# Performance work log

Hardware: AMD Instinct MI355X
Metric: run time of the kernel (lower is better)

The kernel has to match this reference:

```python
import jax, jax.numpy as jnp
import numpy as np

FEATS = 64
POS = 3
EDGE_ATTR = 4
M_DIM = 16
N_LAYERS = 3
EDGE_IN = 2 * FEATS + EDGE_ATTR + 1  # 133


def setup_inputs() -> dict:
    key = jax.random.key(0)
    ks = jax.random.split(key, 20)
    N, E = 50000, 800000
    x = jax.random.normal(ks[0], (N, FEATS + POS), dtype=jnp.float32)
    edge_index = jax.random.randint(ks[1], (2, E), 0, N, dtype=jnp.int64)
    edge_attr = jax.random.normal(ks[2], (E, EDGE_ATTR), dtype=jnp.float32)
    s = 0.02
    L = N_LAYERS
    inp = {
        "x": x, "edge_index": edge_index, "edge_attr": edge_attr,
        # edge_mlp: Linear(EDGE_IN, 2*EDGE_IN) -> SiLU -> Linear(2*EDGE_IN, M_DIM) -> SiLU
        "edge_w1": jax.random.normal(ks[3], (L, EDGE_IN, 2 * EDGE_IN), dtype=jnp.float32) * s,
        "edge_b1": jnp.zeros((L, 2 * EDGE_IN), dtype=jnp.float32),
        "edge_w2": jax.random.normal(ks[4], (L, 2 * EDGE_IN, M_DIM), dtype=jnp.float32) * s,
        "edge_b2": jnp.zeros((L, M_DIM), dtype=jnp.float32),
        # coors_mlp: Linear(M, 4M) -> SiLU -> Linear(4M, 1)
        "coors_w1": jax.random.normal(ks[5], (L, M_DIM, 4 * M_DIM), dtype=jnp.float32) * s,
        "coors_b1": jnp.zeros((L, 4 * M_DIM), dtype=jnp.float32),
        "coors_w2": jax.random.normal(ks[6], (L, 4 * M_DIM, 1), dtype=jnp.float32) * s,
        "coors_b2": jnp.zeros((L, 1), dtype=jnp.float32),
        # node_mlp: Linear(FEATS+M, 2*FEATS) -> SiLU -> Linear(2*FEATS, FEATS)
        "node_w1": jax.random.normal(ks[7], (L, FEATS + M_DIM, 2 * FEATS), dtype=jnp.float32) * s,
        "node_b1": jnp.zeros((L, 2 * FEATS), dtype=jnp.float32),
        "node_w2": jax.random.normal(ks[8], (L, 2 * FEATS, FEATS), dtype=jnp.float32) * s,
        "node_b2": jnp.zeros((L, FEATS), dtype=jnp.float32),
    }
    return inp


def _egnn_layer(x, edge_index, edge_attr,
                ew1, eb1, ew2, eb2, cw1, cb1, cw2, cb2, nw1, nb1, nw2, nb2):
    N = x.shape[0]
    feats, coors = x[:, :FEATS], x[:, FEATS:]
    src, dst = edge_index[0], edge_index[1]
    rel_coors = coors[src] - coors[dst]                       # [E, 3]
    rel_dist = jnp.sum(rel_coors ** 2, axis=-1, keepdims=True)  # [E, 1]
    ea = jnp.concatenate([edge_attr, rel_dist], axis=-1)      # [E, EDGE_ATTR+1]
    # PyG default flow source_to_target: x_i = x[dst], x_j = x[src]
    edge_in = jnp.concatenate([feats[dst], feats[src], ea], axis=-1)  # [E, EDGE_IN]
    h = jax.nn.silu(edge_in @ ew1 + eb1)
    m_ij = jax.nn.silu(h @ ew2 + eb2)                         # [E, M_DIM]
    coor_w = jax.nn.silu(m_ij @ cw1 + cb1) @ cw2 + cb2        # [E, 1]
    # aggregate (default 'add') over destination nodes
    m_i = jax.ops.segment_sum(m_ij, dst, num_segments=N)      # [N, M_DIM]
    coor_wi = jax.ops.segment_sum(coor_w, dst, num_segments=N)  # [N, 1]
    coor_ri = jax.ops.segment_sum(rel_coors, dst, num_segments=N)  # [N, 3]
    coors_out = coors + coor_wi * coor_ri
    node_in = jnp.concatenate([feats, m_i], axis=-1)
    hidden = jax.nn.silu(node_in @ nw1 + nb1) @ nw2 + nb2
    hidden_out = hidden + feats
    return jnp.concatenate([hidden_out, coors_out], axis=-1)


def reference(x, edge_index, edge_attr,
              edge_w1, edge_b1, edge_w2, edge_b2,
              coors_w1, coors_b1, coors_w2, coors_b2,
              node_w1, node_b1, node_w2, node_b2):
    for l in range(N_LAYERS):
        x = _egnn_layer(x, edge_index, edge_attr,
                        edge_w1[l], edge_b1[l], edge_w2[l], edge_b2[l],
                        coors_w1[l], coors_b1[l], coors_w2[l], coors_b2[l],
                        node_w1[l], node_b1[l], node_w2[l], node_b2[l])
    return x
```

## Files before the change

kernel.cpp:

```cpp
#include <hip/hip_runtime.h>
#include <hip/hip_bf16.h>

#define XDIM 67
#define EIN_D 133
#define H1 266
#define KP 160
#define KP_E 168
#define JP 320
#define JP_H 328
#define MSTR 40
#define EPB 48

typedef __attribute__((ext_vector_type(8))) short bf16x8;
typedef __attribute__((ext_vector_type(4))) float f32x4;
typedef __attribute__((ext_vector_type(2))) float f32x2;
typedef __attribute__((ext_vector_type(2))) __bf16 b16x2;

__device__ __forceinline__ float silu_f(float x) {
    return x * __builtin_amdgcn_rcpf(1.f + __expf(-x));
}

__device__ __forceinline__ unsigned short bf16_rne(float f) {
    unsigned int u = __float_as_uint(f);
    u += 0x7fffu + ((u >> 16) & 1u);
    return (unsigned short)(u >> 16);
}
__device__ __forceinline__ float bf16_to_f(unsigned short h) {
    return __uint_as_float(((unsigned int)h) << 16);
}
__device__ __forceinline__ unsigned int packbf2(float a, float b) {
    b16x2 c = __builtin_convertvector((f32x2){a, b}, b16x2);
    unsigned int u; __builtin_memcpy(&u, &c, 4); return u;
}

__global__ void copy_zero_kernel(const float* __restrict__ src, float* __restrict__ dst,
                                 int n, float* __restrict__ z, int nz) {
    int n4 = n >> 2, nz4 = nz >> 2;
    const float4* s4 = (const float4*)src;
    float4* d4 = (float4*)dst;
    float4* z4 = (float4*)z;
    for (int i = blockIdx.x * blockDim.x + threadIdx.x; i < n4; i += gridDim.x * blockDim.x)
        d4[i] = s4[i];
    for (int i = blockIdx.x * blockDim.x + threadIdx.x; i < nz4; i += gridDim.x * blockDim.x)
        z4[i] = make_float4(0.f, 0.f, 0.f, 0.f);
    if (blockIdx.x == 0 && threadIdx.x == 0) {
        for (int i = n4 * 4; i < n; ++i) dst[i] = src[i];
        for (int i = nz4 * 4; i < nz; ++i) z[i] = 0.f;
    }
}

__global__ void prep_w1t(const float* __restrict__ ew1, unsigned short* __restrict__ whi,
                         unsigned short* __restrict__ wlo) {
    int idx = blockIdx.x * 256 + threadIdx.x;
    if (idx >= 3 * JP * KP) return;
    int l = idx / (JP * KP);
    int rem = idx - l * JP * KP;
    int j = rem / KP, k = rem - (rem / KP) * KP;
    float w = (j < H1 && k < EIN_D) ? ew1[((size_t)l * EIN_D + k) * H1 + j] : 0.f;
    unsigned short h = bf16_rne(w);
    whi[idx] = h;
    wlo[idx] = bf16_rne(w - bf16_to_f(h));
}

__global__ void prep_w2t(const float* __restrict__ ew2, unsigned short* __restrict__ w2tg) {
    int idx = blockIdx.x * 256 + threadIdx.x;
    if (idx >= 3 * 16 * JP_H) return;
    int l = idx / (16 * JP_H);
    int rem = idx - l * 16 * JP_H;
    int c = rem / JP_H, j = rem - (rem / JP_H) * JP_H;
    float w = (j < H1) ? ew2[((size_t)l * H1 + j) * 16 + c] : 0.f;
    unsigned short h = bf16_rne(w);
    w2tg[((size_t)l * 2 + 0) * 16 * JP_H + c * JP_H + j] = h;
    w2tg[((size_t)l * 2 + 1) * 16 * JP_H + c * JP_H + j] = bf16_rne(w - bf16_to_f(h));
}

__global__ void prep_b1(const float* __restrict__ b1, float* __restrict__ b1p) {
    int idx = blockIdx.x * 256 + threadIdx.x;
    if (idx >= 3 * JP) return;
    int l = idx / JP, j = idx - (idx / JP) * JP;
    b1p[idx] = (j < H1) ? b1[l * H1 + j] : 0.f;
}

__global__ void prep_cw1t(const float* __restrict__ cw1, unsigned short* __restrict__ cw1t) {
    int idx = blockIdx.x * 256 + threadIdx.x;
    if (idx >= 3 * 64 * 32) return;
    int l = idx / (64 * 32);
    int rem = idx - l * 64 * 32;
    int j = rem >> 5, c = rem & 31;
    cw1t[idx] = (c < 16) ? bf16_rne(cw1[(size_t)l * 16 * 64 + c * 64 + j]) : (unsigned short)0;
}

__device__ __forceinline__ void store_feats(unsigned short* __restrict__ ein_hi,
                                            unsigned short* __restrict__ ein_lo,
                                            int er, int c0, const float* v) {
    unsigned int dh01 = packbf2(v[0], v[1]), dh23 = packbf2(v[2], v[3]);
    unsigned int sh01 = packbf2(v[4], v[5]), sh23 = packbf2(v[6], v[7]);
    float dl0 = v[0] - __uint_as_float(dh01 << 16);
    float dl1 = v[1] - __uint_as_float(dh01 & 0xffff0000u);
    float dl2 = v[2] - __uint_as_float(dh23 << 16);
    float dl3 = v[3] - __uint_as_float(dh23 & 0xffff0000u);
    float sl0 = v[4] - __uint_as_float(sh01 << 16);
    float sl1 = v[5] - __uint_as_float(sh01 & 0xffff0000u);
    float sl2 = v[6] - __uint_as_float(sh23 << 16);
    float sl3 = v[7] - __uint_as_float(sh23 & 0xffff0000u);
    uint2 u;
    u.x = dh01; u.y = dh23;
    *(uint2*)&ein_hi[er * KP_E + c0] = u;
    u.x = packbf2(dl0, dl1); u.y = packbf2(dl2, dl3);
    *(uint2*)&ein_lo[er * KP_E + c0] = u;
    u.x = sh01; u.y = sh23;
    *(uint2*)&ein_hi[er * KP_E + 64 + c0] = u;
    u.x = packbf2(sl0, sl1); u.y = packbf2(sl2, sl3);
    *(uint2*)&ein_lo[er * KP_E + 64 + c0] = u;
}

__global__ __launch_bounds__(256, 4) void edge_kernel(
    const float* __restrict__ x,
    const int* __restrict__ eidx,
    const float* __restrict__ eattr,
    const unsigned short* __restrict__ w1hi,
    const unsigned short* __restrict__ w1lo,
    const float* __restrict__ b1p,
    const unsigned short* __restrict__ w2tg,
    const float* __restrict__ b2,
    const unsigned short* __restrict__ cw1t,
    const float* __restrict__ cb1,
    const float* __restrict__ cw2, const float* __restrict__ cb2,
    float* __restrict__ m_i, float* __restrict__ cri, float* __restrict__ cwi,
    int E, int N)
{
    __shared__ __align__(16) unsigned short uA[2 * EPB * KP_E];
    __shared__ __align__(16) unsigned short mij_bf[EPB * MSTR];
    __shared__ float relc[EPB][4];
    __shared__ int dstl[EPB];

    unsigned short* ein_hi = uA;
    unsigned short* ein_lo = uA + EPB * KP_E;
    unsigned short* h_hi   = uA;

    const int tid = threadIdx.x;
    const int lane = tid & 63;
    const int w = tid >> 6;
    const int ge0 = blockIdx.x * EPB;
    const int r16 = lane & 15, g4 = lane >> 4;

    const int c0 = r16 * 4;
    const int erA = w * 12 + g4, erB = erA + 4, erC = erA + 8;
    const int geA = ge0 + erA, geB = ge0 + erB, geC = ge0 + erC;
    const int sA = (geA < E) ? eidx[geA] : 0, dA = (geA < E) ? eidx[E + geA] : 0;
    const int sB = (geB < E) ? eidx[geB] : 0, dB = (geB < E) ? eidx[E + geB] : 0;
    const int sC = (geC < E) ? eidx[geC] : 0, dC = (geC < E) ? eidx[E + geC] : 0;
    float vA[8], vB[8], vC[8];
    {
        const float* p;
        p = x + (size_t)dA * XDIM + c0; vA[0] = p[0]; vA[1] = p[1]; vA[2] = p[2]; vA[3] = p[3];
        p = x + (size_t)sA * XDIM + c0; vA[4] = p[0]; vA[5] = p[1]; vA[6] = p[2]; vA[7] = p[3];
        p = x + (size_t)dB * XDIM + c0; vB[0] = p[0]; vB[1] = p[1]; vB[2] = p[2]; vB[3] = p[3];
        p = x + (size_t)sB * XDIM + c0; vB[4] = p[0]; vB[5] = p[1]; vB[6] = p[2]; vB[7] = p[3];
        p = x + (size_t)dC * XDIM + c0; vC[0] = p[0]; vC[1] = p[1]; vC[2] = p[2]; vC[3] = p[3];
        p = x + (size_t)sC * XDIM + c0; vC[4] = p[0]; vC[5] = p[1]; vC[6] = p[2]; vC[7] = p[3];
    }

    if (tid < EPB) {
        int e = tid, ge = ge0 + e;
        if (ge < E) {
            int s = eidx[ge];
            int d = eidx[E + ge];
            dstl[e] = d;
            const float* xs = x + (size_t)s * XDIM;
            const float* xd = x + (size_t)d * XDIM;
            float r0 = xs[64] - xd[64], r1 = xs[65] - xd[65], r2 = xs[66] - xd[66];
            relc[e][0] = r0; relc[e][1] = r1; relc[e][2] = r2;
            float dist = r0 * r0 + r1 * r1 + r2 * r2;
            unsigned short hh = bf16_rne(dist);
            ein_hi[e * KP_E + 132] = hh;
            ein_lo[e * KP_E + 132] = bf16_rne(dist - bf16_to_f(hh));
        } else {
            dstl[e] = 0;
            relc[e][0] = relc[e][1] = relc[e][2] = 0.f;
            ein_hi[e * KP_E + 132] = 0;
            ein_lo[e * KP_E + 132] = 0;
        }
    }
    if (tid >= 64) {
        int t = tid - 64;
        int e = t >> 2, c = t & 3, ge = ge0 + e;
        float a = (ge < E) ? eattr[(size_t)ge * 4 + c] : 0.f;
        unsigned short hh = bf16_rne(a);
        ein_hi[e * KP_E + 128 + c] = hh;
        ein_lo[e * KP_E + 128 + c] = bf16_rne(a - bf16_to_f(hh));
    }
    for (int t = tid; t < EPB * 27; t += 256) {
        int e = t / 27, c = 133 + (t - (t / 27) * 27);
        ein_hi[e * KP_E + c] = 0;
        ein_lo[e * KP_E + c] = 0;
    }
    if (tid < 192) {
        int e = tid >> 2, q = tid & 3;
        uint2 zz; zz.x = 0u; zz.y = 0u;
        *(uint2*)&mij_bf[e * MSTR + 16 + q * 4] = zz;
    }

    store_feats(ein_hi, ein_lo, erA, c0, vA);
    store_feats(ein_hi, ein_lo, erB, c0, vB);
    store_feats(ein_hi, ein_lo, erC, c0, vC);
    __syncthreads();

    const int jt0 = w * 5;

    f32x4 acc[5][3];
#pragma unroll
    for (int a = 0; a < 5; ++a)
#pragma unroll
        for (int b = 0; b < 3; ++b) acc[a][b] = (f32x4){0.f, 0.f, 0.f, 0.f};

    __builtin_amdgcn_s_setprio(1);
#pragma unroll
    for (int kk = 0; kk < 5; ++kk) {
        const int ko = kk * 32 + g4 * 8;
        bf16x8 ah[3], al[3];
#pragma unroll
        for (int et = 0; et < 3; ++et) {
            ah[et] = *(const bf16x8*)&ein_hi[(et * 16 + r16) * KP_E + ko];
            al[et] = *(const bf16x8*)&ein_lo[(et * 16 + r16) * KP_E + ko];
        }
#pragma unroll
        for (int j5 = 0; j5 < 5; ++j5) {
            const size_t wo = (size_t)((jt0 + j5) * 16 + r16) * KP + ko;
            bf16x8 bh = *(const bf16x8*)&w1hi[wo];
            bf16x8 bl = *(const bf16x8*)&w1lo[wo];
#pragma unroll
            for (int et = 0; et < 3; ++et) {
                acc[j5][et] = __builtin_amdgcn_mfma_f32_16x16x32_bf16(bh, ah[et], acc[j5][et], 0, 0, 0);
                acc[j5][et] = __builtin_amdgcn_mfma_f32_16x16x32_bf16(bl, ah[et], acc[j5][et], 0, 0, 0);
                acc[j5][et] = __builtin_amdgcn_mfma_f32_16x16x32_bf16(bh, al[et], acc[j5][et], 0, 0, 0);
            }
        }
    }
    __builtin_amdgcn_s_setprio(0);

    float4 b1v[5];
#pragma unroll
    for (int j5 = 0; j5 < 5; ++j5)
        b1v[j5] = *(const float4*)&b1p[(jt0 + j5) * 16 + g4 * 4];

    __syncthreads();

#pragma unroll
    for (int j5 = 0; j5 < 5; ++j5) {
#pragma unroll
        for (int et = 0; et < 3; ++et) {
            f32x4 a = acc[j5][et];
            float h0 = silu_f(a[0] + b1v[j5].x);
            float h1 = silu_f(a[1] + b1v[j5].y);
            float h2 = silu_f(a[2] + b1v[j5].z);
            float h3 = silu_f(a[3] + b1v[j5].w);
            uint2 uu;
            uu.x = packbf2(h0, h1);
            uu.y = packbf2(h2, h3);
            *(uint2*)&h_hi[(et * 16 + r16) * JP_H + (jt0 + j5) * 16 + g4 * 4] = uu;
        }
    }
    __syncthreads();

    if (w < 3) {
        f32x4 acc2 = (f32x4){0.f, 0.f, 0.f, 0.f};
        const unsigned short* hrow = &h_hi[(w * 16 + r16) * JP_H];
        const unsigned short* w2h = &w2tg[(size_t)r16 * JP_H];
        const unsigned short* w2l = &w2tg[(size_t)(16 + r16) * JP_H];
#pragma unroll
        for (int kk = 0; kk < 10; ++kk) {
            const int ko = kk * 32 + g4 * 8;
            bf16x8 hf = *(const bf16x8*)&hrow[ko];
            bf16x8 wh = *(const bf16x8*)&w2h[ko];
            bf16x8 wl = *(const bf16x8*)&w2l[ko];
            acc2 = __builtin_amdgcn_mfma_f32_16x16x32_bf16(hf, wh, acc2, 0, 0, 0);
            acc2 = __builtin_amdgcn_mfma_f32_16x16x32_bf16(hf, wl, acc2, 0, 0, 0);
        }
        float b2v = b2[r16];
#pragma unroll
        for (int r = 0; r < 4; ++r) {
            int e = w * 16 + g4 * 4 + r;
            float m = silu_f(acc2[r] + b2v);
            mij_bf[e * MSTR + r16] = bf16_rne(m);
            if (ge0 + e < E) atomicAdd(&m_i[(size_t)dstl[e] * 16 + r16], m);
        }
    }
    __syncthreads();

    if (w < 3) {
        bf16x8 afrag = *(const bf16x8*)&mij_bf[(w * 16 + r16) * MSTR + g4 * 8];
        f32x4 cacc[4];
#pragma unroll
        for (int jt = 0; jt < 4; ++jt) {
            bf16x8 bfrag = *(const bf16x8*)&cw1t[(jt * 16 + r16) * 32 + g4 * 8];
            cacc[jt] = __builtin_amdgcn_mfma_f32_16x16x32_bf16(afrag, bfrag,
                        (f32x4){0.f, 0.f, 0.f, 0.f}, 0, 0, 0);
        }
        float pw0 = 0.f, pw1 = 0.f, pw2 = 0.f, pw3 = 0.f;
#pragma unroll
        for (int jt = 0; jt < 4; ++jt) {
            float cb = cb1[jt * 16 + r16];
            float cw = cw2[jt * 16 + r16];
            pw0 += silu_f(cacc[jt][0] + cb) * cw;
            pw1 += silu_f(cacc[jt][1] + cb) * cw;
            pw2 += silu_f(cacc[jt][2] + cb) * cw;
            pw3 += silu_f(cacc[jt][3] + cb) * cw;
        }
#pragma unroll
        for (int s = 1; s < 16; s <<= 1) {
            pw0 += __shfl_xor(pw0, s, 16);
            pw1 += __shfl_xor(pw1, s, 16);
            pw2 += __shfl_xor(pw2, s, 16);
            pw3 += __shfl_xor(pw3, s, 16);
        }
        if (r16 == 0) {
            float cb2v = cb2[0];
            int e = w * 16 + g4 * 4;
            relc[e + 0][3] = pw0 + cb2v;
            relc[e + 1][3] = pw1 + cb2v;
            relc[e + 2][3] = pw2 + cb2v;
            relc[e + 3][3] = pw3 + cb2v;
        }
    }
    __syncthreads();

    if (tid < EPB * 4) {
        int e = tid >> 2, c = tid & 3;
        if (ge0 + e < E) {
            int d = dstl[e];
            if (c < 3) atomicAdd(&cri[(size_t)d * 3 + c], relc[e][c]);
            else       atomicAdd(&cwi[d], relc[e][3]);
        }
    }
}

__global__ __launch_bounds__(256) void node_kernel(
    const float* xin,
    float* __restrict__ m_i,
    float* __restrict__ cri,
    float* __restrict__ cwi,
    const float* __restrict__ nw1, const float* __restrict__ nb1,
    const float* __restrict__ nw2, const float* __restrict__ nb2,
    float* xout, int N)
{
    __shared__ __align__(16) float nin[2][80];
    __shared__ __align__(16) float hid[2][128];
    const int half = threadIdx.x >> 7, r = threadIdx.x & 127;
    const int n = blockIdx.x * 2 + half;
    const bool on = (n < N);

    if (on) {
        if (r < 64)      nin[half][r] = xin[(size_t)n * XDIM + r];
        else if (r < 80) nin[half][r] = m_i[(size_t)n * 16 + (r - 64)];
    }
    __syncthreads();
    if (on) {
        float p0 = 0.f, p1 = 0.f, p2 = 0.f, p3 = 0.f;
#pragma unroll
        for (int k = 0; k < 80; k += 16) {
            float4 a0 = *(const float4*)&nin[half][k];
            float4 a1 = *(const float4*)&nin[half][k + 4];
            float4 a2 = *(const float4*)&nin[half][k + 8];
            float4 a3 = *(const float4*)&nin[half][k + 12];
            p0 += a0.x * nw1[(k + 0) * 128 + r] + a0.y * nw1[(k + 1) * 128 + r]
                + a0.z * nw1[(k + 2) * 128 + r] + a0.w * nw1[(k + 3) * 128 + r];
            p1 += a1.x * nw1[(k + 4) * 128 + r] + a1.y * nw1[(k + 5) * 128 + r]
                + a1.z * nw1[(k + 6) * 128 + r] + a1.w * nw1[(k + 7) * 128 + r];
            p2 += a2.x * nw1[(k + 8) * 128 + r] + a2.y * nw1[(k + 9) * 128 + r]
                + a2.z * nw1[(k + 10) * 128 + r] + a2.w * nw1[(k + 11) * 128 + r];
            p3 += a3.x * nw1[(k + 12) * 128 + r] + a3.y * nw1[(k + 13) * 128 + r]
                + a3.z * nw1[(k + 14) * 128 + r] + a3.w * nw1[(k + 15) * 128 + r];
        }
        hid[half][r] = silu_f(nb1[r] + ((p0 + p1) + (p2 + p3)));
    }
    __syncthreads();
    if (on) {
        if (r < 64) {
            float p0 = 0.f, p1 = 0.f, p2 = 0.f, p3 = 0.f;
#pragma unroll
            for (int k = 0; k < 128; k += 16) {
                float4 a0 = *(const float4*)&hid[half][k];
                float4 a1 = *(const float4*)&hid[half][k + 4];
                float4 a2 = *(const float4*)&hid[half][k + 8];
                float4 a3 = *(const float4*)&hid[half][k + 12];
                p0 += a0.x * nw2[(k + 0) * 64 + r] + a0.y * nw2[(k + 1) * 64 + r]
                    + a0.z * nw2[(k + 2) * 64 + r] + a0.w * nw2[(k + 3) * 64 + r];
                p1 += a1.x * nw2[(k + 4) * 64 + r] + a1.y * nw2[(k + 5) * 64 + r]
                    + a1.z * nw2[(k + 6) * 64 + r] + a1.w * nw2[(k + 7) * 64 + r];
                p2 += a2.x * nw2[(k + 8) * 64 + r] + a2.y * nw2[(k + 9) * 64 + r]
                    + a2.z * nw2[(k + 10) * 64 + r] + a2.w * nw2[(k + 11) * 64 + r];
                p3 += a3.x * nw2[(k + 12) * 64 + r] + a3.y * nw2[(k + 13) * 64 + r]
                    + a3.z * nw2[(k + 14) * 64 + r] + a3.w * nw2[(k + 15) * 64 + r];
            }
            xout[(size_t)n * XDIM + r] = nb2[r] + ((p0 + p1) + (p2 + p3)) + nin[half][r];
        } else if (r < 67) {
            int c = r - 64;
            xout[(size_t)n * XDIM + r] =
                xin[(size_t)n * XDIM + r] + cwi[n] * cri[(size_t)n * 3 + c];
        }
    }
    __syncthreads();
    if (on) {
        if (r < 16)      m_i[(size_t)n * 16 + r] = 0.f;
        else if (r < 19) cri[(size_t)n * 3 + (r - 16)] = 0.f;
        else if (r == 19) cwi[n] = 0.f;
    }
}

extern "C" void kernel_launch(void* const* d_in, const int* in_sizes, int n_in,
                              void* d_out, int out_size, void* d_ws, size_t ws_size,
                              hipStream_t stream) {
    const float* x     = (const float*)d_in[0];
    const int*   eidx  = (const int*)d_in[1];
    const float* eattr = (const float*)d_in[2];
    const float* ew1   = (const float*)d_in[3];
    const float* eb1   = (const float*)d_in[4];
    const float* ew2   = (const float*)d_in[5];
    const float* eb2   = (const float*)d_in[6];
    const float* cw1   = (const float*)d_in[7];
    const float* cb1   = (const float*)d_in[8];
    const float* cw2   = (const float*)d_in[9];
    const float* cb2   = (const float*)d_in[10];
    const float* nw1   = (const float*)d_in[11];
    const float* nb1   = (const float*)d_in[12];
    const float* nw2   = (const float*)d_in[13];
    const float* nb2   = (const float*)d_in[14];

    const int N = in_sizes[0] / XDIM;
    const int E = in_sizes[1] / 2;

    float* acc  = (float*)d_ws;
    float* m_i  = acc;
    float* cri  = acc + (size_t)N * 16;
    float* cwi  = acc + (size_t)N * 19;
    float* b1p  = acc + (size_t)N * 20;
    unsigned short* w1hi = (unsigned short*)(b1p + (size_t)3 * JP);
    unsigned short* w1lo = w1hi + (size_t)3 * JP * KP;
    unsigned short* w2tg = w1lo + (size_t)3 * JP * KP;
    unsigned short* cw1t = w2tg + (size_t)3 * 2 * 16 * JP_H;

    float* xwork = (float*)d_out;

    copy_zero_kernel<<<2048, 256, 0, stream>>>(x, xwork, N * XDIM, acc, N * 20);
    prep_w1t<<<(3 * JP * KP + 255) / 256, 256, 0, stream>>>(ew1, w1hi, w1lo);
    prep_w2t<<<(3 * 16 * JP_H + 255) / 256, 256, 0, stream>>>(ew2, w2tg);
    prep_b1<<<(3 * JP + 255) / 256, 256, 0, stream>>>(eb1, b1p);
    prep_cw1t<<<(3 * 64 * 32 + 255) / 256, 256, 0, stream>>>(cw1, cw1t);

    for (int l = 0; l < 3; ++l) {
        edge_kernel<<<(E + EPB - 1) / EPB, 256, 0, stream>>>(
            xwork, eidx, eattr,
            w1hi + (size_t)l * JP * KP, w1lo + (size_t)l * JP * KP,
            b1p + (size_t)l * JP,
            w2tg + (size_t)l * 2 * 16 * JP_H,
            eb2 + (size_t)l * 16,
            cw1t + (size_t)l * 64 * 32,
            cb1 + (size_t)l * 64,
            cw2 + (size_t)l * 64, cb2 + l,
            m_i, cri, cwi, E, N);
        node_kernel<<<(N + 1) / 2, 256, 0, stream>>>(
            xwork, m_i, cri, cwi,
            nw1 + (size_t)l * 80 * 128, nb1 + (size_t)l * 128,
            nw2 + (size_t)l * 128 * 64, nb2 + (size_t)l * 64,
            xwork, N);
    }
}
```

Before: 1.761 ms.

## Sort edges by destination and pre-reduce per-destination runs before atomics

Adds a counting sort of edges by destination node (histogram, single-block scan, scatter into a permutation) once per forward pass. The edge kernel now processes edges in that permuted order and replaces its per-edge atomics with a block-local segmented reduction over runs of equal destination, issuing one atomic per run and channel. The aim is to cut global atomic traffic and contention, and to improve locality of the destination-row gathers. The cost is an extra indirection for edge indices and attributes, the sort kernels including a serial single-block scan, and message sums now built from bf16-rounded m_ij values instead of fp32, which loses precision.

```diff
diff --git a/kernel.cpp b/kernel.cpp
--- a/kernel.cpp
+++ b/kernel.cpp
@@ -49,12 +49,48 @@
     }
 }
 
+__global__ void hist_kernel(const int* __restrict__ eidx, int* __restrict__ cnt, int E) {
+    int i = blockIdx.x * 256 + threadIdx.x;
+    if (i < E) atomicAdd(&cnt[eidx[E + i]], 1);
+}
+
+__global__ __launch_bounds__(256) void scan_kernel(const int* __restrict__ cnt,
+                                                   int* __restrict__ off, int N) {
+    __shared__ int ssum[256];
+    const int tid = threadIdx.x;
+    const int strip = (N + 255) / 256;
+    const int s = tid * strip;
+    const int e = (s + strip < N) ? (s + strip) : N;
+    int acc = 0;
+    for (int i = s; i < e; ++i) acc += cnt[i];
+    ssum[tid] = acc;
+    __syncthreads();
+    for (int d = 1; d < 256; d <<= 1) {
+        int v = (tid >= d) ? ssum[tid - d] : 0;
+        __syncthreads();
+        ssum[tid] += v;
+        __syncthreads();
+    }
+    int base = (tid > 0) ? ssum[tid - 1] : 0;
+    for (int i = s; i < e; ++i) { int c = cnt[i]; off[i] = base; base += c; }
+}
+
+__global__ void scatter_kernel(const int* __restrict__ eidx, int* __restrict__ off,
+                               int* __restrict__ perm, int E) {
+    int i = blockIdx.x * 256 + threadIdx.x;
+    if (i < E) {
+        int d = eidx[E + i];
+        int pos = atomicAdd(&off[d], 1);
+        perm[pos] = i;
+    }
+}
+
 __global__ void prep_w1t(const float* __restrict__ ew1, unsigned short* __restrict__ whi,
                          unsigned short* __restrict__ wlo) {
     int idx = blockIdx.x * 256 + threadIdx.x;
     if (idx >= 3 * JP * KP) return;
     int l = idx / (JP * KP);
-    int rem = idx - l * JP * KP;
+    int rem = idx - l * (JP * KP);
     int j = rem / KP, k = rem - (rem / KP) * KP;
     float w = (j < H1 && k < EIN_D) ? ew1[((size_t)l * EIN_D + k) * H1 + j] : 0.f;
     unsigned short h = bf16_rne(w);
@@ -66,7 +102,7 @@
     int idx = blockIdx.x * 256 + threadIdx.x;
     if (idx >= 3 * 16 * JP_H) return;
     int l = idx / (16 * JP_H);
-    int rem = idx - l * 16 * JP_H;
+    int rem = idx - l * (16 * JP_H);
     int c = rem / JP_H, j = rem - (rem / JP_H) * JP_H;
     float w = (j < H1) ? ew2[((size_t)l * H1 + j) * 16 + c] : 0.f;
     unsigned short h = bf16_rne(w);
@@ -85,7 +121,7 @@
     int idx = blockIdx.x * 256 + threadIdx.x;
     if (idx >= 3 * 64 * 32) return;
     int l = idx / (64 * 32);
-    int rem = idx - l * 64 * 32;
+    int rem = idx - l * (64 * 32);
     int j = rem >> 5, c = rem & 31;
     cw1t[idx] = (c < 16) ? bf16_rne(cw1[(size_t)l * 16 * 64 + c * 64 + j]) : (unsigned short)0;
 }
@@ -117,6 +153,7 @@
 __global__ __launch_bounds__(256, 4) void edge_kernel(
     const float* __restrict__ x,
     const int* __restrict__ eidx,
+    const int* __restrict__ perm,
     const float* __restrict__ eattr,
     const unsigned short* __restrict__ w1hi,
     const unsigned short* __restrict__ w1lo,
@@ -147,9 +184,12 @@
     const int c0 = r16 * 4;
     const int erA = w * 12 + g4, erB = erA + 4, erC = erA + 8;
     const int geA = ge0 + erA, geB = ge0 + erB, geC = ge0 + erC;
-    const int sA = (geA < E) ? eidx[geA] : 0, dA = (geA < E) ? eidx[E + geA] : 0;
-    const int sB = (geB < E) ? eidx[geB] : 0, dB = (geB < E) ? eidx[E + geB] : 0;
-    const int sC = (geC < E) ? eidx[geC] : 0, dC = (geC < E) ? eidx[E + geC] : 0;
+    const int peA = (geA < E) ? perm[geA] : 0;
+    const int peB = (geB < E) ? perm[geB] : 0;
+    const int peC = (geC < E) ? perm[geC] : 0;
+    const int sA = (geA < E) ? eidx[peA] : 0, dA = (geA < E) ? eidx[E + peA] : 0;
+    const int sB = (geB < E) ? eidx[peB] : 0, dB = (geB < E) ? eidx[E + peB] : 0;
+    const int sC = (geC < E) ? eidx[peC] : 0, dC = (geC < E) ? eidx[E + peC] : 0;
     float vA[8], vB[8], vC[8];
     {
         const float* p;
@@ -164,8 +204,9 @@
     if (tid < EPB) {
         int e = tid, ge = ge0 + e;
         if (ge < E) {
-            int s = eidx[ge];
-            int d = eidx[E + ge];
+            int pe = perm[ge];
+            int s = eidx[pe];
+            int d = eidx[E + pe];
             dstl[e] = d;
             const float* xs = x + (size_t)s * XDIM;
             const float* xd = x + (size_t)d * XDIM;
@@ -176,7 +217,7 @@
             ein_hi[e * KP_E + 132] = hh;
             ein_lo[e * KP_E + 132] = bf16_rne(dist - bf16_to_f(hh));
         } else {
-            dstl[e] = 0;
+            dstl[e] = -1;
             relc[e][0] = relc[e][1] = relc[e][2] = 0.f;
             ein_hi[e * KP_E + 132] = 0;
             ein_lo[e * KP_E + 132] = 0;
@@ -185,7 +226,8 @@
     if (tid >= 64) {
         int t = tid - 64;
         int e = t >> 2, c = t & 3, ge = ge0 + e;
-        float a = (ge < E) ? eattr[(size_t)ge * 4 + c] : 0.f;
+        float a = 0.f;
+        if (ge < E) { int pe = perm[ge]; a = eattr[(size_t)pe * 4 + c]; }
         unsigned short hh = bf16_rne(a);
         ein_hi[e * KP_E + 128 + c] = hh;
         ein_lo[e * KP_E + 128 + c] = bf16_rne(a - bf16_to_f(hh));
@@ -283,7 +325,6 @@
             int e = w * 16 + g4 * 4 + r;
             float m = silu_f(acc2[r] + b2v);
             mij_bf[e * MSTR + r16] = bf16_rne(m);
-            if (ge0 + e < E) atomicAdd(&m_i[(size_t)dstl[e] * 16 + r16], m);
         }
     }
     __syncthreads();
@@ -325,12 +366,24 @@
     }
     __syncthreads();
 
-    if (tid < EPB * 4) {
-        int e = tid >> 2, c = tid & 3;
-        if (ge0 + e < E) {
-            int d = dstl[e];
-            if (c < 3) atomicAdd(&cri[(size_t)d * 3 + c], relc[e][c]);
-            else       atomicAdd(&cwi[d], relc[e][3]);
+    for (int it = tid; it < EPB * 20; it += 256) {
+        int e = it / 20, c = it - e * 20;
+        int ge = ge0 + e;
+        if (ge >= E) continue;
+        int d = dstl[e];
+        if (e > 0 && dstl[e - 1] == d) continue;
+        if (c < 16) {
+            float sum = bf16_to_f(mij_bf[e * MSTR + c]);
+            for (int e2 = e + 1; e2 < EPB && ge0 + e2 < E && dstl[e2] == d; ++e2)
+                sum += bf16_to_f(mij_bf[e2 * MSTR + c]);
+            atomicAdd(&m_i[(size_t)d * 16 + c], sum);
+        } else {
+            int cc = c - 16;
+            float sum = relc[e][cc];
+            for (int e2 = e + 1; e2 < EPB && ge0 + e2 < E && dstl[e2] == d; ++e2)
+                sum += relc[e2][cc];
+            if (cc < 3) atomicAdd(&cri[(size_t)d * 3 + cc], sum);
+            else        atomicAdd(&cwi[d], sum);
         }
     }
 }
@@ -434,15 +487,21 @@
     float* m_i  = acc;
     float* cri  = acc + (size_t)N * 16;
     float* cwi  = acc + (size_t)N * 19;
-    float* b1p  = acc + (size_t)N * 20;
+    int*   cnt  = (int*)(acc + (size_t)N * 20);
+    int*   off  = cnt + N;
+    float* b1p  = (float*)(off + N);
     unsigned short* w1hi = (unsigned short*)(b1p + (size_t)3 * JP);
     unsigned short* w1lo = w1hi + (size_t)3 * JP * KP;
     unsigned short* w2tg = w1lo + (size_t)3 * JP * KP;
     unsigned short* cw1t = w2tg + (size_t)3 * 2 * 16 * JP_H;
+    int*   perm = (int*)(cw1t + (size_t)3 * 64 * 32);
 
     float* xwork = (float*)d_out;
 
-    copy_zero_kernel<<<2048, 256, 0, stream>>>(x, xwork, N * XDIM, acc, N * 20);
+    copy_zero_kernel<<<2048, 256, 0, stream>>>(x, xwork, N * XDIM, acc, N * 21);
+    hist_kernel<<<(E + 255) / 256, 256, 0, stream>>>(eidx, cnt, E);
+    scan_kernel<<<1, 256, 0, stream>>>(cnt, off, N);
+    scatter_kernel<<<(E + 255) / 256, 256, 0, stream>>>(eidx, off, perm, E);
     prep_w1t<<<(3 * JP * KP + 255) / 256, 256, 0, stream>>>(ew1, w1hi, w1lo);
     prep_w2t<<<(3 * 16 * JP_H + 255) / 256, 256, 0, stream>>>(ew2, w2tg);
     prep_b1<<<(3 * JP + 255) / 256, 256, 0, stream>>>(eb1, b1p);
@@ -450,7 +509,7 @@
 
     for (int l = 0; l < 3; ++l) {
         edge_kernel<<<(E + EPB - 1) / EPB, 256, 0, stream>>>(
-            xwork, eidx, eattr,
+            xwork, eidx, perm, eattr,
             w1hi + (size_t)l * JP * KP, w1lo + (size_t)l * JP * KP,
             b1p + (size_t)l * JP,
             w2tg + (size_t)l * 2 * 16 * JP_H,
```

Measured after the change: 2.086 ms. 18.4% more time.
